# Performance work log

Measured on AMD Instinct MI355X. Metric: run time of the kernel, lower is better.

## Reference

```python
import jax, jax.numpy as jnp
import numpy as np
import math

NEIGHBOR_RADIUS = 30.0

def _masked_softmax(logits, mask, axis):
    # mask: bool, True = keep; all-masked rows return zeros
    p = jax.nn.softmax(jnp.where(mask, logits, -1e9), axis=axis) * mask.astype(logits.dtype)
    return p / jnp.clip(jnp.sum(p, axis=axis, keepdims=True), 1e-9, None)

def _forward(agents_state, agents_mask, map_polylines, map_poly_mask,
             map_poly_type, map_tl_status, map_on_route,
             pm_w1, pm_b1, pm_w2, pm_b2, type_emb, tl_emb, route_emb,
             mo_w1, mo_b1, mo_w2, mo_b2,
             ae_w1, ae_b1, ae_w2, ae_b2, ae_w3, ae_b3,
             mr_w1, mr_b1, mr_w2, mr_b2,
             nr_w1, nr_b1, nr_w2, nr_b2,
             to_w1, to_b1, to_w2, to_b2):
    relu = jax.nn.relu
    a_mask = (agents_mask > 0.5).astype(agents_state.dtype)   # (B,N,T)
    a_feat = agents_state[..., :5]
    # ---- map polyline node encoder ----
    h = relu(map_polylines @ pm_w1 + pm_b1)                   # (B,M,L,H)
    h = relu(h @ pm_w2 + pm_b2)
    h = h.max(axis=2)                                         # (B,M,H) max-pool over points
    t_idx = jnp.clip(map_poly_type, 0, type_emb.shape[0] - 1)
    s_idx = jnp.clip(map_tl_status, 0, tl_emb.shape[0] - 1)
    r_idx = jnp.clip(map_on_route, 0, route_emb.shape[0] - 1)
    h = h + type_emb[t_idx] + tl_emb[s_idx] + route_emb[r_idx]
    h = relu(h @ mo_w1 + mo_b1) @ mo_w2 + mo_b2
    map_mask = map_poly_mask > 0.5                            # (B,M) bool
    map_node = h * map_mask[..., None].astype(h.dtype)        # (B,M,D)
    map_center = map_polylines.mean(axis=2)                   # (B,M,2)
    # ---- agent state encoder ----
    a = relu(a_feat @ ae_w1 + ae_b1)
    a = relu(a @ ae_w2 + ae_b2)
    a_emb = (a @ ae_w3 + ae_b3) * a_mask[..., None]           # (B,N,T,D)
    D = a_emb.shape[-1]
    # ---- agent -> map attention ----
    agent_pos = a_feat[..., 0:2]
    rel = map_center[:, None, None, :, :] - agent_pos[:, :, :, None, :]  # (B,N,T,M,2)
    dist = jnp.linalg.norm(rel, axis=-1, keepdims=True)
    rel_feat = jnp.concatenate([rel, dist], axis=-1)          # (B,N,T,M,3)
    rel_score = (relu(rel_feat @ mr_w1 + mr_b1) @ mr_w2 + mr_b2)[..., 0]  # (B,N,T,M)
    dot = jnp.einsum('bntd,bmd->bntm', a_emb, map_node) / math.sqrt(D)
    score_mask = jnp.broadcast_to(map_mask[:, None, None, :], dot.shape)
    attn = _masked_softmax(dot + rel_score, score_mask, axis=-1)
    map_ctx = jnp.einsum('bntm,bmd->bntd', attn, map_node)    # (B,N,T,D)
    # ---- neighbor graph attention ----
    pos = a_feat[..., 0:2]
    vel = a_feat[..., 3:5]
    pos_j = jnp.transpose(pos, (0, 2, 1, 3))                  # (B,T,N,2)
    vel_j = jnp.transpose(vel, (0, 2, 1, 3))
    rel_pos = pos_j[:, None, :, :, :] - pos[:, :, :, None, :] # (B,N,T,N,2) = p_j - p_i
    rel_vel = vel_j[:, None, :, :, :] - vel[:, :, :, None, :]
    dist_ij = jnp.linalg.norm(rel_pos, axis=-1, keepdims=True)
    rel_ij = jnp.concatenate([rel_pos, rel_vel, dist_ij], axis=-1)        # (B,N,T,N,5)
    nbr_score = (relu(rel_ij @ nr_w1 + nr_b1) @ nr_w2 + nr_b2)[..., 0]    # (B,N,T,N)
    am_b = agents_mask > 0.5
    valid_i = am_b[..., None]                                 # (B,N,T,1)
    valid_j = jnp.transpose(am_b, (0, 2, 1))[:, None, :, :]   # (B,1,T,N)
    N = pos.shape[1]
    not_self = ~jnp.eye(N, dtype=bool)[None, :, None, :]      # (1,N,1,N)
    nbr_mask = valid_i & valid_j & (dist_ij[..., 0] <= NEIGHBOR_RADIUS) & not_self
    dot_n = jnp.einsum('bitd,bjtd->bitj', a_emb, a_emb) / math.sqrt(D)
    w_n = _masked_softmax(dot_n + nbr_score, nbr_mask, axis=-1)
    nbr_ctx = jnp.einsum('bitj,bjtd->bitd', w_n, a_emb)       # (B,N,T,D)
    # ---- tau head ----
    tau = jnp.concatenate([a_emb, map_ctx, nbr_ctx], axis=-1)
    tau = relu(tau @ to_w1 + to_b1) @ to_w2 + to_b2
    return tau * a_mask[..., None]

def setup_inputs() -> dict:
    key = jax.random.key(0)
    B, N, T, M, L = 2, 32, 32, 256, 20
    H, D, TAU = 128, 128, 64
    ks = jax.random.split(key, 32)
    def f(i, shp):
        return jax.random.normal(ks[i], shp, jnp.float32) * 0.05
    inp = {}
    inp['agents_state'] = jax.random.normal(ks[0], (B, N, T, 5), jnp.float32) * jnp.array([50., 50., 1., 5., 5.], jnp.float32)
    inp['agents_mask'] = jnp.ones((B, N, T), jnp.float32)
    inp['map_polylines'] = jax.random.normal(ks[1], (B, M, L, 2), jnp.float32) * 50.0
    inp['map_poly_mask'] = jnp.ones((B, M), jnp.float32)
    inp['map_poly_type'] = jax.random.randint(ks[2], (B, M), 0, 4)
    inp['map_tl_status'] = jax.random.randint(ks[3], (B, M), 0, 8)
    inp['map_on_route'] = jax.random.randint(ks[4], (B, M), 0, 2)
    inp['pm_w1'] = f(5, (2, H));  inp['pm_b1'] = jnp.zeros((H,), jnp.float32)
    inp['pm_w2'] = f(6, (H, H)); inp['pm_b2'] = jnp.zeros((H,), jnp.float32)
    inp['type_emb'] = f(7, (4, H)); inp['tl_emb'] = f(8, (8, H)); inp['route_emb'] = f(9, (2, H))
    inp['mo_w1'] = f(10, (H, H)); inp['mo_b1'] = jnp.zeros((H,), jnp.float32)
    inp['mo_w2'] = f(11, (H, D)); inp['mo_b2'] = jnp.zeros((D,), jnp.float32)
    inp['ae_w1'] = f(12, (5, H)); inp['ae_b1'] = jnp.zeros((H,), jnp.float32)
    inp['ae_w2'] = f(13, (H, H)); inp['ae_b2'] = jnp.zeros((H,), jnp.float32)
    inp['ae_w3'] = f(14, (H, D)); inp['ae_b3'] = jnp.zeros((D,), jnp.float32)
    inp['mr_w1'] = f(15, (3, H)); inp['mr_b1'] = jnp.zeros((H,), jnp.float32)
    inp['mr_w2'] = f(16, (H, 1)); inp['mr_b2'] = jnp.zeros((1,), jnp.float32)
    inp['nr_w1'] = f(17, (5, H)); inp['nr_b1'] = jnp.zeros((H,), jnp.float32)
    inp['nr_w2'] = f(18, (H, 1)); inp['nr_b2'] = jnp.zeros((1,), jnp.float32)
    inp['to_w1'] = f(19, (3 * D, H)); inp['to_b1'] = jnp.zeros((H,), jnp.float32)
    inp['to_w2'] = f(20, (H, TAU)); inp['to_b2'] = jnp.zeros((TAU,), jnp.float32)
    return inp

def reference(agents_state, agents_mask, map_polylines, map_poly_mask,
              map_poly_type, map_tl_status, map_on_route,
              pm_w1, pm_b1, pm_w2, pm_b2, type_emb, tl_emb, route_emb,
              mo_w1, mo_b1, mo_w2, mo_b2,
              ae_w1, ae_b1, ae_w2, ae_b2, ae_w3, ae_b3,
              mr_w1, mr_b1, mr_w2, mr_b2,
              nr_w1, nr_b1, nr_w2, nr_b2,
              to_w1, to_b1, to_w2, to_b2):
    return _forward(agents_state, agents_mask, map_polylines, map_poly_mask,
                    map_poly_type, map_tl_status, map_on_route,
                    pm_w1, pm_b1, pm_w2, pm_b2, type_emb, tl_emb, route_emb,
                    mo_w1, mo_b1, mo_w2, mo_b2,
                    ae_w1, ae_b1, ae_w2, ae_b2, ae_w3, ae_b3,
                    mr_w1, mr_b1, mr_w2, mr_b2,
                    nr_w1, nr_b1, nr_w2, nr_b2,
                    to_w1, to_b1, to_w2, to_b2)
```

## Files before the change

kernel.cpp:

```cpp
#include <hip/hip_runtime.h>
#include <hip/hip_bf16.h>

#define Bb 2
#define Nn 32
#define Tt 32
#define Mm 256
#define Ll 20
#define Hh 128
#define Dd 128
#define TAUu 64
#define RSQRT_D 0.08838834764831843f

__global__ __launch_bounds__(256) void k_map(
    const float* __restrict__ poly, const float* __restrict__ pmask,
    const int* __restrict__ ptype, const int* __restrict__ ptl, const int* __restrict__ proute,
    const float* __restrict__ pm_w1, const float* __restrict__ pm_b1,
    const float* __restrict__ pm_w2, const float* __restrict__ pm_b2,
    const float* __restrict__ type_emb, const float* __restrict__ tl_emb, const float* __restrict__ route_emb,
    const float* __restrict__ mo_w1, const float* __restrict__ mo_b1,
    const float* __restrict__ mo_w2, const float* __restrict__ mo_b2,
    float* __restrict__ map_node, float* __restrict__ map_nodeT, float* __restrict__ map_center)
{
    int bm = blockIdx.x;
    int b  = bm >> 8;
    int m  = bm & 255;
    int tid = threadIdx.x;
    int h    = tid & 127;
    int half = tid >> 7;
    __shared__ float pts[Ll*2];
    __shared__ float h1a[Ll][Hh];
    __shared__ float hv[Hh];
    __shared__ float red[Hh];
    if (tid < Ll*2) pts[tid] = poly[bm*Ll*2 + tid];
    __syncthreads();
    float w1x = pm_w1[h];
    float w1y = pm_w1[Hh+h];
    float bb1 = pm_b1[h];
    int l0 = half*10;
    #pragma unroll
    for (int u = 0; u < 10; ++u) {
        int l = l0 + u;
        h1a[l][h] = fmaxf(fmaf(w1x, pts[2*l], fmaf(w1y, pts[2*l+1], bb1)), 0.f);
    }
    __syncthreads();
    float bb2 = pm_b2[h];
    float acc[10];
    #pragma unroll
    for (int u = 0; u < 10; ++u) acc[u] = bb2;
    for (int k = 0; k < Hh; ++k) {
        float w = pm_w2[k*Hh + h];
        #pragma unroll
        for (int u = 0; u < 10; ++u) acc[u] = fmaf(h1a[l0+u][k], w, acc[u]);
    }
    float mx = 0.f;
    #pragma unroll
    for (int u = 0; u < 10; ++u) mx = fmaxf(mx, acc[u]);
    if (half == 1) red[h] = mx;
    __syncthreads();
    if (half == 0) {
        float mm2 = fmaxf(mx, red[h]);
        int ti = min(max(ptype[bm], 0), 3);
        int si = min(max(ptl[bm], 0), 7);
        int ri = min(max(proute[bm], 0), 1);
        hv[h] = mm2 + type_emb[ti*Hh+h] + tl_emb[si*Hh+h] + route_emb[ri*Hh+h];
    }
    __syncthreads();
    float a1 = 0.f;
    for (int k = half*64; k < half*64 + 64; ++k) a1 = fmaf(hv[k], mo_w1[k*Hh+h], a1);
    if (half == 1) red[h] = a1;
    __syncthreads();
    if (half == 0) hv[h] = fmaxf(a1 + red[h] + mo_b1[h], 0.f);
    __syncthreads();
    float a2 = 0.f;
    for (int k = half*64; k < half*64 + 64; ++k) a2 = fmaf(hv[k], mo_w2[k*Dd+h], a2);
    if (half == 1) red[h] = a2;
    __syncthreads();
    if (half == 0) {
        float val = a2 + red[h] + mo_b2[h];
        float mk = (pmask[bm] > 0.5f) ? 1.f : 0.f;
        val *= mk;
        map_node[bm*Dd + h] = val;
        map_nodeT[(b*Dd + h)*Mm + m] = val;
    }
    if (tid == 0) {
        float sx = 0.f, sy = 0.f;
        for (int l = 0; l < Ll; ++l) { sx += pts[2*l]; sy += pts[2*l+1]; }
        map_center[bm*2+0] = sx / (float)Ll;
        map_center[bm*2+1] = sy / (float)Ll;
    }
}

__global__ __launch_bounds__(128) void k_agent(
    const float* __restrict__ astate, const float* __restrict__ amask,
    const float* __restrict__ ae_w1, const float* __restrict__ ae_b1,
    const float* __restrict__ ae_w2, const float* __restrict__ ae_b2,
    const float* __restrict__ ae_w3, const float* __restrict__ ae_b3,
    float* __restrict__ a_emb)
{
    int r0 = blockIdx.x * 4;
    int h  = threadIdx.x;
    __shared__ float f5[4][5];
    __shared__ float a1s[4][Hh];
    if (h < 20) f5[h/5][h%5] = astate[(r0 + h/5)*5 + (h%5)];
    __syncthreads();
    float acc[4];
    float b1v = ae_b1[h];
    #pragma unroll
    for (int r = 0; r < 4; ++r) acc[r] = b1v;
    #pragma unroll
    for (int k = 0; k < 5; ++k) {
        float w = ae_w1[k*Hh + h];
        #pragma unroll
        for (int r = 0; r < 4; ++r) acc[r] = fmaf(f5[r][k], w, acc[r]);
    }
    #pragma unroll
    for (int r = 0; r < 4; ++r) a1s[r][h] = fmaxf(acc[r], 0.f);
    __syncthreads();
    float b2v = ae_b2[h];
    #pragma unroll
    for (int r = 0; r < 4; ++r) acc[r] = b2v;
    for (int k = 0; k < Hh; ++k) {
        float w = ae_w2[k*Hh + h];
        #pragma unroll
        for (int r = 0; r < 4; ++r) acc[r] = fmaf(a1s[r][k], w, acc[r]);
    }
    float v2[4];
    #pragma unroll
    for (int r = 0; r < 4; ++r) v2[r] = fmaxf(acc[r], 0.f);
    __syncthreads();
    #pragma unroll
    for (int r = 0; r < 4; ++r) a1s[r][h] = v2[r];
    __syncthreads();
    float b3v = ae_b3[h];
    #pragma unroll
    for (int r = 0; r < 4; ++r) acc[r] = b3v;
    for (int k = 0; k < Hh; ++k) {
        float w = ae_w3[k*Dd + h];
        #pragma unroll
        for (int r = 0; r < 4; ++r) acc[r] = fmaf(a1s[r][k], w, acc[r]);
    }
    #pragma unroll
    for (int r = 0; r < 4; ++r) {
        float mk = (amask[r0+r] > 0.5f) ? 1.f : 0.f;
        a_emb[(r0+r)*Dd + h] = acc[r] * mk;
    }
}

__global__ __launch_bounds__(256) void k_mapattn(
    const float* __restrict__ astate, const float* __restrict__ pmask,
    const float* __restrict__ a_emb, const float* __restrict__ map_node,
    const float* __restrict__ map_nodeT, const float* __restrict__ map_center,
    const float* __restrict__ mr_w1, const float* __restrict__ mr_b1,
    const float* __restrict__ mr_w2, const float* __restrict__ mr_b2,
    float* __restrict__ map_ctx)
{
    int r0  = blockIdx.x * 4;
    int b   = r0 >> 10;
    int tid = threadIdx.x;
    __shared__ float w1m[3*Hh];
    __shared__ float b1m[Hh];
    __shared__ float w2m[Hh];
    __shared__ float pxy4[4][2];
    __shared__ float ae4[4][Dd];
    __shared__ float lg4[4][Mm];
    __shared__ float redc[4][Dd];
    for (int q = tid; q < 3*Hh; q += 256) w1m[q] = mr_w1[q];
    if (tid < Hh) { b1m[tid] = mr_b1[tid]; w2m[tid] = mr_w2[tid]; }
    for (int q = tid; q < 512; q += 256) ae4[q>>7][q&127] = a_emb[(r0 + (q>>7))*Dd + (q&127)];
    if (tid < 8) pxy4[tid>>1][tid&1] = astate[(r0 + (tid>>1))*5 + (tid&1)];
    float b2c = mr_b2[0];
    __syncthreads();

    {
        int m = tid;
        float cx = map_center[(b*Mm+m)*2+0];
        float cy = map_center[(b*Mm+m)*2+1];
        float rx[4], ry[4], dv[4], sA[4], dt[4];
        #pragma unroll
        for (int r = 0; r < 4; ++r) {
            rx[r] = cx - pxy4[r][0];
            ry[r] = cy - pxy4[r][1];
            dv[r] = sqrtf(rx[r]*rx[r] + ry[r]*ry[r]);
            sA[r] = b2c;
            dt[r] = 0.f;
        }
        for (int hh = 0; hh < Hh; ++hh) {
            float wa = w1m[hh], wb = w1m[Hh+hh], wc = w1m[2*Hh+hh];
            float bbv = b1m[hh], w2v = w2m[hh];
            #pragma unroll
            for (int r = 0; r < 4; ++r) {
                float t1 = fmaxf(fmaf(rx[r], wa, fmaf(ry[r], wb, fmaf(dv[r], wc, bbv))), 0.f);
                sA[r] = fmaf(t1, w2v, sA[r]);
            }
        }
        for (int d = 0; d < Dd; ++d) {
            float v = map_nodeT[(b*Dd + d)*Mm + m];
            #pragma unroll
            for (int r = 0; r < 4; ++r) dt[r] = fmaf(ae4[r][d], v, dt[r]);
        }
        bool mk = pmask[b*Mm+m] > 0.5f;
        #pragma unroll
        for (int r = 0; r < 4; ++r)
            lg4[r][m] = mk ? fmaf(dt[r], RSQRT_D, sA[r]) : -1e30f;
    }
    __syncthreads();

    {
        int w = tid >> 6, lam = tid & 63;
        float x0 = lg4[w][lam], x1 = lg4[w][64+lam], x2 = lg4[w][128+lam], x3 = lg4[w][192+lam];
        float mxv = fmaxf(fmaxf(x0,x1), fmaxf(x2,x3));
        for (int off = 32; off; off >>= 1) mxv = fmaxf(mxv, __shfl_xor(mxv, off));
        float e0 = (x0 > -1e29f) ? expf(x0-mxv) : 0.f;
        float e1 = (x1 > -1e29f) ? expf(x1-mxv) : 0.f;
        float e2 = (x2 > -1e29f) ? expf(x2-mxv) : 0.f;
        float e3 = (x3 > -1e29f) ? expf(x3-mxv) : 0.f;
        float sm = e0+e1+e2+e3;
        for (int off = 32; off; off >>= 1) sm += __shfl_xor(sm, off);
        float inv = 1.f / fmaxf(sm, 1e-9f);
        lg4[w][lam]     = e0*inv;
        lg4[w][64+lam]  = e1*inv;
        lg4[w][128+lam] = e2*inv;
        lg4[w][192+lam] = e3*inv;
    }
    __syncthreads();

    {
        int d = tid & 127, hf = tid >> 7;
        float acc[4] = {0.f, 0.f, 0.f, 0.f};
        for (int mm = 0; mm < 128; ++mm) {
            int m2 = (hf<<7) + mm;
            float v = map_node[(b*Mm+m2)*Dd + d];
            #pragma unroll
            for (int r = 0; r < 4; ++r) acc[r] = fmaf(lg4[r][m2], v, acc[r]);
        }
        if (hf == 1) {
            #pragma unroll
            for (int r = 0; r < 4; ++r) redc[r][d] = acc[r];
        }
        __syncthreads();
        if (hf == 0) {
            #pragma unroll
            for (int r = 0; r < 4; ++r) map_ctx[(r0+r)*Dd + d] = acc[r] + redc[r][d];
        }
    }
}

__global__ __launch_bounds__(256) void k_nbr_out(
    const float* __restrict__ astate, const float* __restrict__ amask,
    const float* __restrict__ a_emb, const float* __restrict__ map_ctx,
    const float* __restrict__ nr_w1, const float* __restrict__ nr_b1,
    const float* __restrict__ nr_w2, const float* __restrict__ nr_b2,
    const float* __restrict__ to_w1, const float* __restrict__ to_b1,
    const float* __restrict__ to_w2, const float* __restrict__ to_b2,
    float* __restrict__ out)
{
    int r0 = blockIdx.x * 4;
    int b  = r0 >> 10;
    int i  = (r0 >> 5) & 31;
    int t0 = r0 & 31;
    int tid = threadIdx.x;
    __shared__ float w1n[5*Hh];
    __shared__ float b1n[Hh];
    __shared__ float w2n[Hh];
    __shared__ float ei4[4][Dd];
    __shared__ float tau[4][3*Dd];
    __shared__ float jdat[4][Nn][5];
    __shared__ float rowdat[4][5];
    __shared__ float lgn[4][Nn];
    __shared__ float g1s[4][Hh];
    __shared__ float redn[4][Dd];

    for (int q = tid; q < 5*Hh; q += 256) w1n[q] = nr_w1[q];
    if (tid < Hh) { b1n[tid] = nr_b1[tid]; w2n[tid] = nr_w2[tid]; }
    for (int q = tid; q < 512; q += 256) {
        int rr = q>>7, d = q&127;
        float v = a_emb[(r0+rr)*Dd + d];
        ei4[rr][d] = v;
        tau[rr][d] = v;
        tau[rr][Dd + d] = map_ctx[(r0+rr)*Dd + d];
    }
    if (tid < 128) {
        int rr = tid >> 5, j = tid & 31;
        int rj = ((b*Nn + j)*Tt + t0 + rr);
        jdat[rr][j][0] = astate[rj*5+0];
        jdat[rr][j][1] = astate[rj*5+1];
        jdat[rr][j][2] = astate[rj*5+3];
        jdat[rr][j][3] = astate[rj*5+4];
        jdat[rr][j][4] = amask[rj];
    }
    if (tid < 4) {
        int ri_ = r0 + tid;
        rowdat[tid][0] = astate[ri_*5+0];
        rowdat[tid][1] = astate[ri_*5+1];
        rowdat[tid][2] = astate[ri_*5+3];
        rowdat[tid][3] = astate[ri_*5+4];
        rowdat[tid][4] = amask[ri_];
    }
    float b2c = nr_b2[0];
    __syncthreads();

    {
        int j = tid >> 3, c = tid & 7;
        float mlp[4], dtn[4], ddv[4];
        #pragma unroll
        for (int r = 0; r < 4; ++r) {
            float rpx = jdat[r][j][0] - rowdat[r][0];
            float rpy = jdat[r][j][1] - rowdat[r][1];
            float rvx = jdat[r][j][2] - rowdat[r][2];
            float rvy = jdat[r][j][3] - rowdat[r][3];
            float dd = sqrtf(rpx*rpx + rpy*rpy);
            int rj = ((b*Nn + j)*Tt + t0 + r);
            const float* ej = a_emb + (size_t)rj*Dd;
            float am = 0.f, ad = 0.f;
            #pragma unroll 4
            for (int u = 0; u < 16; ++u) {
                int hh = (u<<3) + c;
                float t1 = fmaf(rpx, w1n[hh], fmaf(rpy, w1n[Hh+hh],
                           fmaf(rvx, w1n[2*Hh+hh], fmaf(rvy, w1n[3*Hh+hh],
                           fmaf(dd,  w1n[4*Hh+hh], b1n[hh])))));
                t1 = fmaxf(t1, 0.f);
                am = fmaf(t1, w2n[hh], am);
                ad = fmaf(ei4[r][hh], ej[hh], ad);
            }
            am += __shfl_xor(am, 1); ad += __shfl_xor(ad, 1);
            am += __shfl_xor(am, 2); ad += __shfl_xor(ad, 2);
            am += __shfl_xor(am, 4); ad += __shfl_xor(ad, 4);
            mlp[r] = am; dtn[r] = ad; ddv[r] = dd;
        }
        if (c == 0) {
            #pragma unroll
            for (int r = 0; r < 4; ++r) {
                bool vi = rowdat[r][4] > 0.5f;
                bool vj = jdat[r][j][4] > 0.5f;
                bool ok = vi && vj && (ddv[r] <= 30.0f) && (j != i);
                lgn[r][j] = ok ? fmaf(dtn[r], RSQRT_D, b2c + mlp[r]) : -1e30f;
            }
        }
    }
    __syncthreads();

    {
        int w = tid >> 6, lam = tid & 63;
        float x = (lam < Nn) ? lgn[w][lam] : -1e30f;
        float mxv = x;
        for (int off = 32; off; off >>= 1) mxv = fmaxf(mxv, __shfl_xor(mxv, off));
        float e = (x > -1e29f) ? expf(x - mxv) : 0.f;
        float sm = e;
        for (int off = 32; off; off >>= 1) sm += __shfl_xor(sm, off);
        float inv = 1.f / fmaxf(sm, 1e-9f);
        if (lam < Nn) lgn[w][lam] = e * inv;
    }
    __syncthreads();

    {
        int d = tid & 127, hf = tid >> 7;
        float acc[4] = {0.f,0.f,0.f,0.f};
        for (int jj = 0; jj < 16; ++jj) {
            int j2 = (hf<<4) + jj;
            #pragma unroll
            for (int r = 0; r < 4; ++r) {
                float v = a_emb[((size_t)((b*Nn + j2)*Tt + t0 + r))*Dd + d];
                acc[r] = fmaf(lgn[r][j2], v, acc[r]);
            }
        }
        if (hf == 1) {
            #pragma unroll
            for (int r = 0; r < 4; ++r) redn[r][d] = acc[r];
        }
        __syncthreads();
        if (hf == 0) {
            #pragma unroll
            for (int r = 0; r < 4; ++r) tau[r][2*Dd + d] = acc[r] + redn[r][d];
        }
    }
    __syncthreads();

    {
        int h = tid & 127, rp = tid >> 7;
        float accA = 0.f, accB = 0.f;
        for (int k = 0; k < 3*Dd; ++k) {
            float w = to_w1[k*Hh + h];
            accA = fmaf(tau[rp][k],   w, accA);
            accB = fmaf(tau[rp+2][k], w, accB);
        }
        float bv = to_b1[h];
        g1s[rp][h]   = fmaxf(accA + bv, 0.f);
        g1s[rp+2][h] = fmaxf(accB + bv, 0.f);
    }
    __syncthreads();

    {
        int o = tid & 63, row = tid >> 6;
        float acc = to_b2[o];
        for (int hh = 0; hh < Hh; ++hh) acc = fmaf(g1s[row][hh], to_w2[hh*TAUu + o], acc);
        float vi = (rowdat[row][4] > 0.5f) ? 1.f : 0.f;
        out[(r0+row)*TAUu + o] = acc * vi;
    }
}

extern "C" void kernel_launch(void* const* d_in, const int* in_sizes, int n_in,
                              void* d_out, int out_size, void* d_ws, size_t ws_size,
                              hipStream_t stream) {
    const float* agents_state  = (const float*)d_in[0];
    const float* agents_mask   = (const float*)d_in[1];
    const float* map_polylines = (const float*)d_in[2];
    const float* map_poly_mask = (const float*)d_in[3];
    const int*   map_poly_type = (const int*)d_in[4];
    const int*   map_tl_status = (const int*)d_in[5];
    const int*   map_on_route  = (const int*)d_in[6];
    const float* pm_w1 = (const float*)d_in[7];
    const float* pm_b1 = (const float*)d_in[8];
    const float* pm_w2 = (const float*)d_in[9];
    const float* pm_b2 = (const float*)d_in[10];
    const float* type_emb  = (const float*)d_in[11];
    const float* tl_emb    = (const float*)d_in[12];
    const float* route_emb = (const float*)d_in[13];
    const float* mo_w1 = (const float*)d_in[14];
    const float* mo_b1 = (const float*)d_in[15];
    const float* mo_w2 = (const float*)d_in[16];
    const float* mo_b2 = (const float*)d_in[17];
    const float* ae_w1 = (const float*)d_in[18];
    const float* ae_b1 = (const float*)d_in[19];
    const float* ae_w2 = (const float*)d_in[20];
    const float* ae_b2 = (const float*)d_in[21];
    const float* ae_w3 = (const float*)d_in[22];
    const float* ae_b3 = (const float*)d_in[23];
    const float* mr_w1 = (const float*)d_in[24];
    const float* mr_b1 = (const float*)d_in[25];
    const float* mr_w2 = (const float*)d_in[26];
    const float* mr_b2 = (const float*)d_in[27];
    const float* nr_w1 = (const float*)d_in[28];
    const float* nr_b1 = (const float*)d_in[29];
    const float* nr_w2 = (const float*)d_in[30];
    const float* nr_b2 = (const float*)d_in[31];
    const float* to_w1 = (const float*)d_in[32];
    const float* to_b1 = (const float*)d_in[33];
    const float* to_w2 = (const float*)d_in[34];
    const float* to_b2 = (const float*)d_in[35];

    float* ws = (float*)d_ws;
    float* map_node   = ws;
    float* map_nodeT  = ws + 65536;
    float* map_center = ws + 131072;
    float* a_emb      = ws + 132096;
    float* map_ctx    = ws + 394240;

    float* out = (float*)d_out;

    k_map<<<Bb*Mm, 256, 0, stream>>>(map_polylines, map_poly_mask,
        map_poly_type, map_tl_status, map_on_route,
        pm_w1, pm_b1, pm_w2, pm_b2, type_emb, tl_emb, route_emb,
        mo_w1, mo_b1, mo_w2, mo_b2, map_node, map_nodeT, map_center);

    k_agent<<<Bb*Nn*Tt/4, 128, 0, stream>>>(agents_state, agents_mask,
        ae_w1, ae_b1, ae_w2, ae_b2, ae_w3, ae_b3, a_emb);

    k_mapattn<<<Bb*Nn*Tt/4, 256, 0, stream>>>(agents_state, map_poly_mask,
        a_emb, map_node, map_nodeT, map_center, mr_w1, mr_b1, mr_w2, mr_b2, map_ctx);

    k_nbr_out<<<Bb*Nn*Tt/4, 256, 0, stream>>>(agents_state, agents_mask,
        a_emb, map_ctx, nr_w1, nr_b1, nr_w2, nr_b2,
        to_w1, to_b1, to_w2, to_b2, out);
}
```

Measured before the change: 202.4 us.

## Restructure pipeline into five kernels with split polyline MLP and merged attention

The map encoder is split in two. A fully parallel elementwise kernel computes the first polyline layer and the centers into a global buffer, and a second kernel does the second layer with register-blocked weights, the max-pool and the output MLP. Map attention and neighbor-score computation are merged into one launch with extra blocks, and the output MLP is split across four k-slices with float4 shared loads. Together these aim to raise parallelism and cut serial per-block work. The cost is a large intermediate buffer written and read through global memory, plus extra global traffic for the neighbor probabilities.

```diff
diff --git a/kernel.cpp b/kernel.cpp
--- a/kernel.cpp
+++ b/kernel.cpp
@@ -1,96 +1,30 @@
 #include <hip/hip_runtime.h>
-#include <hip/hip_bf16.h>
-
-#define Bb 2
-#define Nn 32
-#define Tt 32
-#define Mm 256
-#define Ll 20
-#define Hh 128
-#define Dd 128
-#define TAUu 64
+
 #define RSQRT_D 0.08838834764831843f
 
-__global__ __launch_bounds__(256) void k_map(
-    const float* __restrict__ poly, const float* __restrict__ pmask,
-    const int* __restrict__ ptype, const int* __restrict__ ptl, const int* __restrict__ proute,
+__global__ __launch_bounds__(256) void k1_poly(
+    const float* __restrict__ poly,
     const float* __restrict__ pm_w1, const float* __restrict__ pm_b1,
-    const float* __restrict__ pm_w2, const float* __restrict__ pm_b2,
-    const float* __restrict__ type_emb, const float* __restrict__ tl_emb, const float* __restrict__ route_emb,
-    const float* __restrict__ mo_w1, const float* __restrict__ mo_b1,
-    const float* __restrict__ mo_w2, const float* __restrict__ mo_b2,
-    float* __restrict__ map_node, float* __restrict__ map_nodeT, float* __restrict__ map_center)
+    float* __restrict__ h1g, float* __restrict__ center)
 {
-    int bm = blockIdx.x;
-    int b  = bm >> 8;
-    int m  = bm & 255;
-    int tid = threadIdx.x;
-    int h    = tid & 127;
-    int half = tid >> 7;
-    __shared__ float pts[Ll*2];
-    __shared__ float h1a[Ll][Hh];
-    __shared__ float hv[Hh];
-    __shared__ float red[Hh];
-    if (tid < Ll*2) pts[tid] = poly[bm*Ll*2 + tid];
-    __syncthreads();
-    float w1x = pm_w1[h];
-    float w1y = pm_w1[Hh+h];
-    float bb1 = pm_b1[h];
-    int l0 = half*10;
-    #pragma unroll
-    for (int u = 0; u < 10; ++u) {
-        int l = l0 + u;
-        h1a[l][h] = fmaxf(fmaf(w1x, pts[2*l], fmaf(w1y, pts[2*l+1], bb1)), 0.f);
-    }
-    __syncthreads();
-    float bb2 = pm_b2[h];
-    float acc[10];
-    #pragma unroll
-    for (int u = 0; u < 10; ++u) acc[u] = bb2;
-    for (int k = 0; k < Hh; ++k) {
-        float w = pm_w2[k*Hh + h];
-        #pragma unroll
-        for (int u = 0; u < 10; ++u) acc[u] = fmaf(h1a[l0+u][k], w, acc[u]);
-    }
-    float mx = 0.f;
-    #pragma unroll
-    for (int u = 0; u < 10; ++u) mx = fmaxf(mx, acc[u]);
-    if (half == 1) red[h] = mx;
-    __syncthreads();
-    if (half == 0) {
-        float mm2 = fmaxf(mx, red[h]);
-        int ti = min(max(ptype[bm], 0), 3);
-        int si = min(max(ptl[bm], 0), 7);
-        int ri = min(max(proute[bm], 0), 1);
-        hv[h] = mm2 + type_emb[ti*Hh+h] + tl_emb[si*Hh+h] + route_emb[ri*Hh+h];
-    }
-    __syncthreads();
-    float a1 = 0.f;
-    for (int k = half*64; k < half*64 + 64; ++k) a1 = fmaf(hv[k], mo_w1[k*Hh+h], a1);
-    if (half == 1) red[h] = a1;
-    __syncthreads();
-    if (half == 0) hv[h] = fmaxf(a1 + red[h] + mo_b1[h], 0.f);
-    __syncthreads();
-    float a2 = 0.f;
-    for (int k = half*64; k < half*64 + 64; ++k) a2 = fmaf(hv[k], mo_w2[k*Dd+h], a2);
-    if (half == 1) red[h] = a2;
-    __syncthreads();
-    if (half == 0) {
-        float val = a2 + red[h] + mo_b2[h];
-        float mk = (pmask[bm] > 0.5f) ? 1.f : 0.f;
-        val *= mk;
-        map_node[bm*Dd + h] = val;
-        map_nodeT[(b*Dd + h)*Mm + m] = val;
-    }
-    if (tid == 0) {
-        float sx = 0.f, sy = 0.f;
-        for (int l = 0; l < Ll; ++l) { sx += pts[2*l]; sy += pts[2*l+1]; }
-        map_center[bm*2+0] = sx / (float)Ll;
-        map_center[bm*2+1] = sy / (float)Ll;
-    }
-}
-
-__global__ __launch_bounds__(128) void k_agent(
+    int idx = blockIdx.x * 256 + threadIdx.x;
+    if (blockIdx.x < 5120) {
+        int row = idx >> 7, k = idx & 127;
+        float x = poly[row*2], y = poly[row*2+1];
+        h1g[idx] = fmaxf(fmaf(x, pm_w1[k], fmaf(y, pm_w1[128+k], pm_b1[k])), 0.f);
+    } else {
+        int p = idx - 5120*256;
+        if (p < 512) {
+            float sx = 0.f, sy = 0.f;
+            #pragma unroll
+            for (int l = 0; l < 20; ++l) { sx += poly[p*40 + 2*l]; sy += poly[p*40 + 2*l + 1]; }
+            center[p*2+0] = sx * 0.05f;
+            center[p*2+1] = sy * 0.05f;
+        }
+    }
+}
+
+__global__ __launch_bounds__(128) void k2_agent(
     const float* __restrict__ astate, const float* __restrict__ amask,
     const float* __restrict__ ae_w1, const float* __restrict__ ae_b1,
     const float* __restrict__ ae_w2, const float* __restrict__ ae_b2,
@@ -98,303 +32,361 @@
     float* __restrict__ a_emb)
 {
     int r0 = blockIdx.x * 4;
-    int h  = threadIdx.x;
+    int h = threadIdx.x;
     __shared__ float f5[4][5];
-    __shared__ float a1s[4][Hh];
+    __shared__ __align__(16) float a1s[4][128];
     if (h < 20) f5[h/5][h%5] = astate[(r0 + h/5)*5 + (h%5)];
     __syncthreads();
-    float acc[4];
     float b1v = ae_b1[h];
+    float v[4];
+    {
+        float w0 = ae_w1[h], w1 = ae_w1[128+h], w2 = ae_w1[256+h], w3 = ae_w1[384+h], w4 = ae_w1[512+h];
+        #pragma unroll
+        for (int r = 0; r < 4; ++r) {
+            float a = b1v;
+            a = fmaf(f5[r][0], w0, a); a = fmaf(f5[r][1], w1, a);
+            a = fmaf(f5[r][2], w2, a); a = fmaf(f5[r][3], w3, a);
+            a = fmaf(f5[r][4], w4, a);
+            v[r] = fmaxf(a, 0.f);
+        }
+    }
     #pragma unroll
-    for (int r = 0; r < 4; ++r) acc[r] = b1v;
+    for (int r = 0; r < 4; ++r) a1s[r][h] = v[r];
+    __syncthreads();
+    {
+        float b2v = ae_b2[h];
+        float a0 = b2v, a1 = b2v, a2 = b2v, a3 = b2v;
+        for (int kc = 0; kc < 32; ++kc) {
+            float4 x0 = *(const float4*)&a1s[0][kc*4];
+            float4 x1 = *(const float4*)&a1s[1][kc*4];
+            float4 x2 = *(const float4*)&a1s[2][kc*4];
+            float4 x3 = *(const float4*)&a1s[3][kc*4];
+            float w0 = ae_w2[(kc*4+0)*128+h], w1 = ae_w2[(kc*4+1)*128+h];
+            float w2 = ae_w2[(kc*4+2)*128+h], w3 = ae_w2[(kc*4+3)*128+h];
+            a0 = fmaf(x0.x,w0,fmaf(x0.y,w1,fmaf(x0.z,w2,fmaf(x0.w,w3,a0))));
+            a1 = fmaf(x1.x,w0,fmaf(x1.y,w1,fmaf(x1.z,w2,fmaf(x1.w,w3,a1))));
+            a2 = fmaf(x2.x,w0,fmaf(x2.y,w1,fmaf(x2.z,w2,fmaf(x2.w,w3,a2))));
+            a3 = fmaf(x3.x,w0,fmaf(x3.y,w1,fmaf(x3.z,w2,fmaf(x3.w,w3,a3))));
+        }
+        v[0]=fmaxf(a0,0.f); v[1]=fmaxf(a1,0.f); v[2]=fmaxf(a2,0.f); v[3]=fmaxf(a3,0.f);
+    }
+    __syncthreads();
     #pragma unroll
-    for (int k = 0; k < 5; ++k) {
-        float w = ae_w1[k*Hh + h];
-        #pragma unroll
-        for (int r = 0; r < 4; ++r) acc[r] = fmaf(f5[r][k], w, acc[r]);
-    }
-    #pragma unroll
-    for (int r = 0; r < 4; ++r) a1s[r][h] = fmaxf(acc[r], 0.f);
-    __syncthreads();
-    float b2v = ae_b2[h];
-    #pragma unroll
-    for (int r = 0; r < 4; ++r) acc[r] = b2v;
-    for (int k = 0; k < Hh; ++k) {
-        float w = ae_w2[k*Hh + h];
-        #pragma unroll
-        for (int r = 0; r < 4; ++r) acc[r] = fmaf(a1s[r][k], w, acc[r]);
-    }
-    float v2[4];
-    #pragma unroll
-    for (int r = 0; r < 4; ++r) v2[r] = fmaxf(acc[r], 0.f);
-    __syncthreads();
-    #pragma unroll
-    for (int r = 0; r < 4; ++r) a1s[r][h] = v2[r];
-    __syncthreads();
-    float b3v = ae_b3[h];
-    #pragma unroll
-    for (int r = 0; r < 4; ++r) acc[r] = b3v;
-    for (int k = 0; k < Hh; ++k) {
-        float w = ae_w3[k*Dd + h];
-        #pragma unroll
-        for (int r = 0; r < 4; ++r) acc[r] = fmaf(a1s[r][k], w, acc[r]);
+    for (int r = 0; r < 4; ++r) a1s[r][h] = v[r];
+    __syncthreads();
+    {
+        float b3v = ae_b3[h];
+        float a0 = b3v, a1 = b3v, a2 = b3v, a3 = b3v;
+        for (int kc = 0; kc < 32; ++kc) {
+            float4 x0 = *(const float4*)&a1s[0][kc*4];
+            float4 x1 = *(const float4*)&a1s[1][kc*4];
+            float4 x2 = *(const float4*)&a1s[2][kc*4];
+            float4 x3 = *(const float4*)&a1s[3][kc*4];
+            float w0 = ae_w3[(kc*4+0)*128+h], w1 = ae_w3[(kc*4+1)*128+h];
+            float w2 = ae_w3[(kc*4+2)*128+h], w3 = ae_w3[(kc*4+3)*128+h];
+            a0 = fmaf(x0.x,w0,fmaf(x0.y,w1,fmaf(x0.z,w2,fmaf(x0.w,w3,a0))));
+            a1 = fmaf(x1.x,w0,fmaf(x1.y,w1,fmaf(x1.z,w2,fmaf(x1.w,w3,a1))));
+            a2 = fmaf(x2.x,w0,fmaf(x2.y,w1,fmaf(x2.z,w2,fmaf(x2.w,w3,a2))));
+            a3 = fmaf(x3.x,w0,fmaf(x3.y,w1,fmaf(x3.z,w2,fmaf(x3.w,w3,a3))));
+        }
+        v[0]=a0; v[1]=a1; v[2]=a2; v[3]=a3;
     }
     #pragma unroll
     for (int r = 0; r < 4; ++r) {
         float mk = (amask[r0+r] > 0.5f) ? 1.f : 0.f;
-        a_emb[(r0+r)*Dd + h] = acc[r] * mk;
-    }
-}
-
-__global__ __launch_bounds__(256) void k_mapattn(
-    const float* __restrict__ astate, const float* __restrict__ pmask,
+        a_emb[(r0+r)*128 + h] = v[r] * mk;
+    }
+}
+
+__global__ __launch_bounds__(128) void k3_mapnode(
+    const float* __restrict__ h1g, const float* __restrict__ pmask,
+    const int* __restrict__ ptype, const int* __restrict__ ptl, const int* __restrict__ proute,
+    const float* __restrict__ pm_w2, const float* __restrict__ pm_b2,
+    const float* __restrict__ type_emb, const float* __restrict__ tl_emb, const float* __restrict__ route_emb,
+    const float* __restrict__ mo_w1, const float* __restrict__ mo_b1,
+    const float* __restrict__ mo_w2, const float* __restrict__ mo_b2,
+    float* __restrict__ map_node, float* __restrict__ map_nodeT)
+{
+    int bm = blockIdx.x;
+    int b = bm >> 8, m = bm & 255;
+    int h = threadIdx.x;
+    __shared__ __align__(16) float hv[128];
+    __shared__ __align__(16) float g2[128];
+    float acc[20];
+    #pragma unroll
+    for (int l = 0; l < 20; ++l) acc[l] = 0.f;
+    for (int kc = 0; kc < 8; ++kc) {
+        float w[16];
+        #pragma unroll
+        for (int i = 0; i < 16; ++i) w[i] = pm_w2[(kc*16+i)*128 + h];
+        const float* hb = h1g + bm*2560 + kc*16;
+        #pragma unroll
+        for (int l = 0; l < 20; ++l) {
+            const float* xl = hb + l*128;
+            #pragma unroll
+            for (int i = 0; i < 16; ++i) acc[l] = fmaf(xl[i], w[i], acc[l]);
+        }
+    }
+    float mx = acc[0];
+    #pragma unroll
+    for (int l = 1; l < 20; ++l) mx = fmaxf(mx, acc[l]);
+    float val = fmaxf(mx + pm_b2[h], 0.f);
+    int ti = min(max(ptype[bm],0),3);
+    int si = min(max(ptl[bm],0),7);
+    int ri = min(max(proute[bm],0),1);
+    hv[h] = val + type_emb[ti*128+h] + tl_emb[si*128+h] + route_emb[ri*128+h];
+    __syncthreads();
+    float a1 = mo_b1[h];
+    for (int kc = 0; kc < 32; ++kc) {
+        float4 xv = *(const float4*)&hv[kc*4];
+        a1 = fmaf(xv.x, mo_w1[(kc*4+0)*128+h],
+             fmaf(xv.y, mo_w1[(kc*4+1)*128+h],
+             fmaf(xv.z, mo_w1[(kc*4+2)*128+h],
+             fmaf(xv.w, mo_w1[(kc*4+3)*128+h], a1))));
+    }
+    g2[h] = fmaxf(a1, 0.f);
+    __syncthreads();
+    float a2 = mo_b2[h];
+    for (int kc = 0; kc < 32; ++kc) {
+        float4 xv = *(const float4*)&g2[kc*4];
+        a2 = fmaf(xv.x, mo_w2[(kc*4+0)*128+h],
+             fmaf(xv.y, mo_w2[(kc*4+1)*128+h],
+             fmaf(xv.z, mo_w2[(kc*4+2)*128+h],
+             fmaf(xv.w, mo_w2[(kc*4+3)*128+h], a2))));
+    }
+    float mk = (pmask[bm] > 0.5f) ? 1.f : 0.f;
+    a2 *= mk;
+    map_node[bm*128 + h] = a2;
+    map_nodeT[(b*128+h)*256 + m] = a2;
+}
+
+__global__ __launch_bounds__(256) void k4_attn(
+    const float* __restrict__ astate, const float* __restrict__ amask,
+    const float* __restrict__ pmask,
     const float* __restrict__ a_emb, const float* __restrict__ map_node,
-    const float* __restrict__ map_nodeT, const float* __restrict__ map_center,
+    const float* __restrict__ map_nodeT, const float* __restrict__ center,
     const float* __restrict__ mr_w1, const float* __restrict__ mr_b1,
     const float* __restrict__ mr_w2, const float* __restrict__ mr_b2,
-    float* __restrict__ map_ctx)
+    const float* __restrict__ nr_w1, const float* __restrict__ nr_b1,
+    const float* __restrict__ nr_w2, const float* __restrict__ nr_b2,
+    float* __restrict__ map_ctx, float* __restrict__ p_n)
 {
-    int r0  = blockIdx.x * 4;
-    int b   = r0 >> 10;
     int tid = threadIdx.x;
-    __shared__ float w1m[3*Hh];
-    __shared__ float b1m[Hh];
-    __shared__ float w2m[Hh];
-    __shared__ float pxy4[4][2];
-    __shared__ float ae4[4][Dd];
-    __shared__ float lg4[4][Mm];
-    __shared__ float redc[4][Dd];
-    for (int q = tid; q < 3*Hh; q += 256) w1m[q] = mr_w1[q];
-    if (tid < Hh) { b1m[tid] = mr_b1[tid]; w2m[tid] = mr_w2[tid]; }
-    for (int q = tid; q < 512; q += 256) ae4[q>>7][q&127] = a_emb[(r0 + (q>>7))*Dd + (q&127)];
-    if (tid < 8) pxy4[tid>>1][tid&1] = astate[(r0 + (tid>>1))*5 + (tid&1)];
-    float b2c = mr_b2[0];
-    __syncthreads();
-
-    {
+    int lam = tid & 63, wv = tid >> 6;
+    __shared__ float lg4[4][256];
+    __shared__ __align__(16) float p4[256*4];
+    __shared__ float ctxp[4][128];
+
+    if (blockIdx.x < 512) {
+        int r0 = blockIdx.x * 4;
+        int b = r0 >> 10;
         int m = tid;
-        float cx = map_center[(b*Mm+m)*2+0];
-        float cy = map_center[(b*Mm+m)*2+1];
-        float rx[4], ry[4], dv[4], sA[4], dt[4];
+        float rx[4], ry[4], dd[4], dt[4], sA[4];
+        float b2c = mr_b2[0];
+        float cx = center[(b*256+m)*2+0], cy = center[(b*256+m)*2+1];
         #pragma unroll
         for (int r = 0; r < 4; ++r) {
-            rx[r] = cx - pxy4[r][0];
-            ry[r] = cy - pxy4[r][1];
-            dv[r] = sqrtf(rx[r]*rx[r] + ry[r]*ry[r]);
-            sA[r] = b2c;
-            dt[r] = 0.f;
-        }
-        for (int hh = 0; hh < Hh; ++hh) {
-            float wa = w1m[hh], wb = w1m[Hh+hh], wc = w1m[2*Hh+hh];
-            float bbv = b1m[hh], w2v = w2m[hh];
+            float px = astate[(r0+r)*5+0], py = astate[(r0+r)*5+1];
+            rx[r] = cx - px; ry[r] = cy - py;
+            dd[r] = sqrtf(rx[r]*rx[r] + ry[r]*ry[r]);
+            dt[r] = 0.f; sA[r] = b2c;
+        }
+        #pragma unroll 8
+        for (int hh = 0; hh < 128; ++hh) {
+            float wa = mr_w1[hh], wb = mr_w1[128+hh], wc = mr_w1[256+hh];
+            float bb = mr_b1[hh], w2 = mr_w2[hh];
             #pragma unroll
             for (int r = 0; r < 4; ++r) {
-                float t1 = fmaxf(fmaf(rx[r], wa, fmaf(ry[r], wb, fmaf(dv[r], wc, bbv))), 0.f);
-                sA[r] = fmaf(t1, w2v, sA[r]);
+                float t1 = fmaf(rx[r], wa, fmaf(ry[r], wb, fmaf(dd[r], wc, bb)));
+                sA[r] = fmaf(fmaxf(t1, 0.f), w2, sA[r]);
             }
         }
-        for (int d = 0; d < Dd; ++d) {
-            float v = map_nodeT[(b*Dd + d)*Mm + m];
-            #pragma unroll
-            for (int r = 0; r < 4; ++r) dt[r] = fmaf(ae4[r][d], v, dt[r]);
-        }
-        bool mk = pmask[b*Mm+m] > 0.5f;
+        const float* mT = map_nodeT + b*128*256 + m;
+        #pragma unroll 8
+        for (int d = 0; d < 128; ++d) {
+            float v = mT[d*256];
+            #pragma unroll
+            for (int r = 0; r < 4; ++r)
+                dt[r] = fmaf(v, a_emb[(r0+r)*128 + d], dt[r]);
+        }
+        bool mk = pmask[b*256+m] > 0.5f;
         #pragma unroll
         for (int r = 0; r < 4; ++r)
             lg4[r][m] = mk ? fmaf(dt[r], RSQRT_D, sA[r]) : -1e30f;
-    }
-    __syncthreads();
-
-    {
-        int w = tid >> 6, lam = tid & 63;
-        float x0 = lg4[w][lam], x1 = lg4[w][64+lam], x2 = lg4[w][128+lam], x3 = lg4[w][192+lam];
-        float mxv = fmaxf(fmaxf(x0,x1), fmaxf(x2,x3));
-        for (int off = 32; off; off >>= 1) mxv = fmaxf(mxv, __shfl_xor(mxv, off));
-        float e0 = (x0 > -1e29f) ? expf(x0-mxv) : 0.f;
-        float e1 = (x1 > -1e29f) ? expf(x1-mxv) : 0.f;
-        float e2 = (x2 > -1e29f) ? expf(x2-mxv) : 0.f;
-        float e3 = (x3 > -1e29f) ? expf(x3-mxv) : 0.f;
-        float sm = e0+e1+e2+e3;
-        for (int off = 32; off; off >>= 1) sm += __shfl_xor(sm, off);
-        float inv = 1.f / fmaxf(sm, 1e-9f);
-        lg4[w][lam]     = e0*inv;
-        lg4[w][64+lam]  = e1*inv;
-        lg4[w][128+lam] = e2*inv;
-        lg4[w][192+lam] = e3*inv;
-    }
-    __syncthreads();
-
-    {
-        int d = tid & 127, hf = tid >> 7;
-        float acc[4] = {0.f, 0.f, 0.f, 0.f};
-        for (int mm = 0; mm < 128; ++mm) {
-            int m2 = (hf<<7) + mm;
-            float v = map_node[(b*Mm+m2)*Dd + d];
-            #pragma unroll
-            for (int r = 0; r < 4; ++r) acc[r] = fmaf(lg4[r][m2], v, acc[r]);
-        }
-        if (hf == 1) {
-            #pragma unroll
-            for (int r = 0; r < 4; ++r) redc[r][d] = acc[r];
-        }
         __syncthreads();
-        if (hf == 0) {
-            #pragma unroll
-            for (int r = 0; r < 4; ++r) map_ctx[(r0+r)*Dd + d] = acc[r] + redc[r][d];
-        }
-    }
-}
-
-__global__ __launch_bounds__(256) void k_nbr_out(
-    const float* __restrict__ astate, const float* __restrict__ amask,
-    const float* __restrict__ a_emb, const float* __restrict__ map_ctx,
-    const float* __restrict__ nr_w1, const float* __restrict__ nr_b1,
-    const float* __restrict__ nr_w2, const float* __restrict__ nr_b2,
+        {
+            float x0 = lg4[wv][lam], x1 = lg4[wv][64+lam], x2 = lg4[wv][128+lam], x3 = lg4[wv][192+lam];
+            float mxv = fmaxf(fmaxf(x0,x1), fmaxf(x2,x3));
+            #pragma unroll
+            for (int off = 32; off; off >>= 1) mxv = fmaxf(mxv, __shfl_xor(mxv, off));
+            float e0 = (x0 > -1e29f) ? expf(x0-mxv) : 0.f;
+            float e1 = (x1 > -1e29f) ? expf(x1-mxv) : 0.f;
+            float e2 = (x2 > -1e29f) ? expf(x2-mxv) : 0.f;
+            float e3 = (x3 > -1e29f) ? expf(x3-mxv) : 0.f;
+            float sm = e0+e1+e2+e3;
+            #pragma unroll
+            for (int off = 32; off; off >>= 1) sm += __shfl_xor(sm, off);
+            float inv = 1.f / fmaxf(sm, 1e-9f);
+            p4[lam*4 + wv]       = e0*inv;
+            p4[(64+lam)*4 + wv]  = e1*inv;
+            p4[(128+lam)*4 + wv] = e2*inv;
+            p4[(192+lam)*4 + wv] = e3*inv;
+        }
+        __syncthreads();
+        {
+            int d = tid & 127, hf = tid >> 7;
+            float ac0 = 0.f, ac1 = 0.f, ac2 = 0.f, ac3 = 0.f;
+            const float* mn = map_node + (b*256 + hf*128)*128 + d;
+            const float4* pp = (const float4*)p4 + hf*128;
+            #pragma unroll 4
+            for (int mm = 0; mm < 128; ++mm) {
+                float4 pv = pp[mm];
+                float v = mn[mm*128];
+                ac0 = fmaf(pv.x, v, ac0); ac1 = fmaf(pv.y, v, ac1);
+                ac2 = fmaf(pv.z, v, ac2); ac3 = fmaf(pv.w, v, ac3);
+            }
+            if (hf == 1) { ctxp[0][d]=ac0; ctxp[1][d]=ac1; ctxp[2][d]=ac2; ctxp[3][d]=ac3; }
+            __syncthreads();
+            if (hf == 0) {
+                map_ctx[(r0+0)*128+d] = ac0 + ctxp[0][d];
+                map_ctx[(r0+1)*128+d] = ac1 + ctxp[1][d];
+                map_ctx[(r0+2)*128+d] = ac2 + ctxp[2][d];
+                map_ctx[(r0+3)*128+d] = ac3 + ctxp[3][d];
+            }
+        }
+    } else {
+        int rA = (blockIdx.x - 512)*8 + wv*2;
+        int hf = lam >> 5, j = lam & 31;
+        int r = rA + hf;
+        int b = r >> 10, ii = (r >> 5) & 31, tt = r & 31;
+        int rj = (b*32 + j)*32 + tt;
+        float pxi = astate[r*5+0], pyi = astate[r*5+1], vxi = astate[r*5+3], vyi = astate[r*5+4];
+        float pxj = astate[rj*5+0], pyj = astate[rj*5+1], vxj = astate[rj*5+3], vyj = astate[rj*5+4];
+        float rpx = pxj-pxi, rpy = pyj-pyi, rvx = vxj-vxi, rvy = vyj-vyi;
+        float ddv = sqrtf(rpx*rpx + rpy*rpy);
+        float acc = nr_b2[0], dot = 0.f;
+        const float* ei = a_emb + (size_t)r*128;
+        const float* ej = a_emb + (size_t)rj*128;
+        #pragma unroll 8
+        for (int hh = 0; hh < 128; ++hh) {
+            float wA = nr_w1[hh], wB = nr_w1[128+hh], wC = nr_w1[256+hh];
+            float wD = nr_w1[384+hh], wE = nr_w1[512+hh];
+            float bb = nr_b1[hh], w2 = nr_w2[hh];
+            float t1 = fmaf(rpx, wA, fmaf(rpy, wB, fmaf(rvx, wC,
+                       fmaf(rvy, wD, fmaf(ddv, wE, bb)))));
+            acc = fmaf(fmaxf(t1, 0.f), w2, acc);
+            dot = fmaf(ei[hh], ej[hh], dot);
+        }
+        bool vi = amask[r] > 0.5f, vj = amask[rj] > 0.5f;
+        bool ok = vi && vj && (ddv <= 30.0f) && (j != ii);
+        float lg = ok ? fmaf(dot, RSQRT_D, acc) : -1e30f;
+        float mxv = lg;
+        #pragma unroll
+        for (int off = 16; off; off >>= 1) mxv = fmaxf(mxv, __shfl_xor(mxv, off));
+        float e = (lg > -1e29f) ? expf(lg - mxv) : 0.f;
+        float sm = e;
+        #pragma unroll
+        for (int off = 16; off; off >>= 1) sm += __shfl_xor(sm, off);
+        p_n[r*32 + j] = e / fmaxf(sm, 1e-9f);
+    }
+}
+
+__global__ __launch_bounds__(256) void k5_out(
+    const float* __restrict__ amask, const float* __restrict__ a_emb,
+    const float* __restrict__ map_ctx, const float* __restrict__ p_n,
     const float* __restrict__ to_w1, const float* __restrict__ to_b1,
     const float* __restrict__ to_w2, const float* __restrict__ to_b2,
     float* __restrict__ out)
 {
     int r0 = blockIdx.x * 4;
-    int b  = r0 >> 10;
-    int i  = (r0 >> 5) & 31;
-    int t0 = r0 & 31;
+    int b = r0 >> 10, t0 = r0 & 31;
     int tid = threadIdx.x;
-    __shared__ float w1n[5*Hh];
-    __shared__ float b1n[Hh];
-    __shared__ float w2n[Hh];
-    __shared__ float ei4[4][Dd];
-    __shared__ float tau[4][3*Dd];
-    __shared__ float jdat[4][Nn][5];
-    __shared__ float rowdat[4][5];
-    __shared__ float lgn[4][Nn];
-    __shared__ float g1s[4][Hh];
-    __shared__ float redn[4][Dd];
-
-    for (int q = tid; q < 5*Hh; q += 256) w1n[q] = nr_w1[q];
-    if (tid < Hh) { b1n[tid] = nr_b1[tid]; w2n[tid] = nr_w2[tid]; }
+    __shared__ __align__(16) float tau[4][384];
+    __shared__ float redn[4][128];
+    __shared__ __align__(16) float gpart[4][4][128];
+    __shared__ __align__(16) float g1s[4][128];
+
     for (int q = tid; q < 512; q += 256) {
-        int rr = q>>7, d = q&127;
-        float v = a_emb[(r0+rr)*Dd + d];
-        ei4[rr][d] = v;
-        tau[rr][d] = v;
-        tau[rr][Dd + d] = map_ctx[(r0+rr)*Dd + d];
-    }
-    if (tid < 128) {
-        int rr = tid >> 5, j = tid & 31;
-        int rj = ((b*Nn + j)*Tt + t0 + rr);
-        jdat[rr][j][0] = astate[rj*5+0];
-        jdat[rr][j][1] = astate[rj*5+1];
-        jdat[rr][j][2] = astate[rj*5+3];
-        jdat[rr][j][3] = astate[rj*5+4];
-        jdat[rr][j][4] = amask[rj];
-    }
-    if (tid < 4) {
-        int ri_ = r0 + tid;
-        rowdat[tid][0] = astate[ri_*5+0];
-        rowdat[tid][1] = astate[ri_*5+1];
-        rowdat[tid][2] = astate[ri_*5+3];
-        rowdat[tid][3] = astate[ri_*5+4];
-        rowdat[tid][4] = amask[ri_];
-    }
-    float b2c = nr_b2[0];
-    __syncthreads();
-
-    {
-        int j = tid >> 3, c = tid & 7;
-        float mlp[4], dtn[4], ddv[4];
-        #pragma unroll
-        for (int r = 0; r < 4; ++r) {
-            float rpx = jdat[r][j][0] - rowdat[r][0];
-            float rpy = jdat[r][j][1] - rowdat[r][1];
-            float rvx = jdat[r][j][2] - rowdat[r][2];
-            float rvy = jdat[r][j][3] - rowdat[r][3];
-            float dd = sqrtf(rpx*rpx + rpy*rpy);
-            int rj = ((b*Nn + j)*Tt + t0 + r);
-            const float* ej = a_emb + (size_t)rj*Dd;
-            float am = 0.f, ad = 0.f;
-            #pragma unroll 4
-            for (int u = 0; u < 16; ++u) {
-                int hh = (u<<3) + c;
-                float t1 = fmaf(rpx, w1n[hh], fmaf(rpy, w1n[Hh+hh],
-                           fmaf(rvx, w1n[2*Hh+hh], fmaf(rvy, w1n[3*Hh+hh],
-                           fmaf(dd,  w1n[4*Hh+hh], b1n[hh])))));
-                t1 = fmaxf(t1, 0.f);
-                am = fmaf(t1, w2n[hh], am);
-                ad = fmaf(ei4[r][hh], ej[hh], ad);
-            }
-            am += __shfl_xor(am, 1); ad += __shfl_xor(ad, 1);
-            am += __shfl_xor(am, 2); ad += __shfl_xor(ad, 2);
-            am += __shfl_xor(am, 4); ad += __shfl_xor(ad, 4);
-            mlp[r] = am; dtn[r] = ad; ddv[r] = dd;
-        }
-        if (c == 0) {
-            #pragma unroll
-            for (int r = 0; r < 4; ++r) {
-                bool vi = rowdat[r][4] > 0.5f;
-                bool vj = jdat[r][j][4] > 0.5f;
-                bool ok = vi && vj && (ddv[r] <= 30.0f) && (j != i);
-                lgn[r][j] = ok ? fmaf(dtn[r], RSQRT_D, b2c + mlp[r]) : -1e30f;
-            }
-        }
-    }
-    __syncthreads();
-
-    {
-        int w = tid >> 6, lam = tid & 63;
-        float x = (lam < Nn) ? lgn[w][lam] : -1e30f;
-        float mxv = x;
-        for (int off = 32; off; off >>= 1) mxv = fmaxf(mxv, __shfl_xor(mxv, off));
-        float e = (x > -1e29f) ? expf(x - mxv) : 0.f;
-        float sm = e;
-        for (int off = 32; off; off >>= 1) sm += __shfl_xor(sm, off);
-        float inv = 1.f / fmaxf(sm, 1e-9f);
-        if (lam < Nn) lgn[w][lam] = e * inv;
-    }
-    __syncthreads();
-
+        int rr = q >> 7, d = q & 127;
+        tau[rr][d]       = a_emb[(r0+rr)*128 + d];
+        tau[rr][128 + d] = map_ctx[(r0+rr)*128 + d];
+    }
+    __syncthreads();
     {
         int d = tid & 127, hf = tid >> 7;
-        float acc[4] = {0.f,0.f,0.f,0.f};
+        float ac[4] = {0.f,0.f,0.f,0.f};
         for (int jj = 0; jj < 16; ++jj) {
-            int j2 = (hf<<4) + jj;
-            #pragma unroll
-            for (int r = 0; r < 4; ++r) {
-                float v = a_emb[((size_t)((b*Nn + j2)*Tt + t0 + r))*Dd + d];
-                acc[r] = fmaf(lgn[r][j2], v, acc[r]);
-            }
-        }
-        if (hf == 1) {
-            #pragma unroll
-            for (int r = 0; r < 4; ++r) redn[r][d] = acc[r];
-        }
+            int j2 = hf*16 + jj;
+            float p0 = p_n[(r0+0)*32 + j2];
+            float p1 = p_n[(r0+1)*32 + j2];
+            float p2 = p_n[(r0+2)*32 + j2];
+            float p3 = p_n[(r0+3)*32 + j2];
+            const float* ejb = a_emb + (size_t)((b*32 + j2)*32 + t0)*128 + d;
+            ac[0] = fmaf(p0, ejb[0],     ac[0]);
+            ac[1] = fmaf(p1, ejb[128],   ac[1]);
+            ac[2] = fmaf(p2, ejb[256],   ac[2]);
+            ac[3] = fmaf(p3, ejb[384],   ac[3]);
+        }
+        if (hf == 1) { redn[0][d]=ac[0]; redn[1][d]=ac[1]; redn[2][d]=ac[2]; redn[3][d]=ac[3]; }
         __syncthreads();
         if (hf == 0) {
             #pragma unroll
-            for (int r = 0; r < 4; ++r) tau[r][2*Dd + d] = acc[r] + redn[r][d];
-        }
-    }
-    __syncthreads();
-
+            for (int r = 0; r < 4; ++r) tau[r][256 + d] = ac[r] + redn[r][d];
+        }
+    }
+    __syncthreads();
+    {
+        int h6 = tid & 63, kq = tid >> 6;
+        float aL[4] = {0.f,0.f,0.f,0.f};
+        float aH[4] = {0.f,0.f,0.f,0.f};
+        for (int c = 0; c < 24; ++c) {
+            int k4 = kq*24 + c;
+            float4 x0 = *(const float4*)&tau[0][k4*4];
+            float4 x1 = *(const float4*)&tau[1][k4*4];
+            float4 x2 = *(const float4*)&tau[2][k4*4];
+            float4 x3 = *(const float4*)&tau[3][k4*4];
+            float wl0 = to_w1[(k4*4+0)*128 + h6],    wh0 = to_w1[(k4*4+0)*128 + 64+h6];
+            float wl1 = to_w1[(k4*4+1)*128 + h6],    wh1 = to_w1[(k4*4+1)*128 + 64+h6];
+            float wl2 = to_w1[(k4*4+2)*128 + h6],    wh2 = to_w1[(k4*4+2)*128 + 64+h6];
+            float wl3 = to_w1[(k4*4+3)*128 + h6],    wh3 = to_w1[(k4*4+3)*128 + 64+h6];
+            aL[0]=fmaf(x0.x,wl0,fmaf(x0.y,wl1,fmaf(x0.z,wl2,fmaf(x0.w,wl3,aL[0]))));
+            aH[0]=fmaf(x0.x,wh0,fmaf(x0.y,wh1,fmaf(x0.z,wh2,fmaf(x0.w,wh3,aH[0]))));
+            aL[1]=fmaf(x1.x,wl0,fmaf(x1.y,wl1,fmaf(x1.z,wl2,fmaf(x1.w,wl3,aL[1]))));
+            aH[1]=fmaf(x1.x,wh0,fmaf(x1.y,wh1,fmaf(x1.z,wh2,fmaf(x1.w,wh3,aH[1]))));
+            aL[2]=fmaf(x2.x,wl0,fmaf(x2.y,wl1,fmaf(x2.z,wl2,fmaf(x2.w,wl3,aL[2]))));
+            aH[2]=fmaf(x2.x,wh0,fmaf(x2.y,wh1,fmaf(x2.z,wh2,fmaf(x2.w,wh3,aH[2]))));
+            aL[3]=fmaf(x3.x,wl0,fmaf(x3.y,wl1,fmaf(x3.z,wl2,fmaf(x3.w,wl3,aL[3]))));
+            aH[3]=fmaf(x3.x,wh0,fmaf(x3.y,wh1,fmaf(x3.z,wh2,fmaf(x3.w,wh3,aH[3]))));
+        }
+        #pragma unroll
+        for (int r = 0; r < 4; ++r) {
+            gpart[kq][r][h6]      = aL[r];
+            gpart[kq][r][64 + h6] = aH[r];
+        }
+    }
+    __syncthreads();
     {
         int h = tid & 127, rp = tid >> 7;
-        float accA = 0.f, accB = 0.f;
-        for (int k = 0; k < 3*Dd; ++k) {
-            float w = to_w1[k*Hh + h];
-            accA = fmaf(tau[rp][k],   w, accA);
-            accB = fmaf(tau[rp+2][k], w, accB);
-        }
         float bv = to_b1[h];
-        g1s[rp][h]   = fmaxf(accA + bv, 0.f);
-        g1s[rp+2][h] = fmaxf(accB + bv, 0.f);
-    }
-    __syncthreads();
-
+        #pragma unroll
+        for (int rr = rp; rr < 4; rr += 2) {
+            float s = gpart[0][rr][h] + gpart[1][rr][h] + gpart[2][rr][h] + gpart[3][rr][h];
+            g1s[rr][h] = fmaxf(s + bv, 0.f);
+        }
+    }
+    __syncthreads();
     {
         int o = tid & 63, row = tid >> 6;
-        float acc = to_b2[o];
-        for (int hh = 0; hh < Hh; ++hh) acc = fmaf(g1s[row][hh], to_w2[hh*TAUu + o], acc);
-        float vi = (rowdat[row][4] > 0.5f) ? 1.f : 0.f;
-        out[(r0+row)*TAUu + o] = acc * vi;
+        float a2 = to_b2[o];
+        for (int kc = 0; kc < 32; ++kc) {
+            float4 g = *(const float4*)&g1s[row][kc*4];
+            a2 = fmaf(g.x, to_w2[(kc*4+0)*64 + o],
+                 fmaf(g.y, to_w2[(kc*4+1)*64 + o],
+                 fmaf(g.z, to_w2[(kc*4+2)*64 + o],
+                 fmaf(g.w, to_w2[(kc*4+3)*64 + o], a2))));
+        }
+        float mk = (amask[r0+row] > 0.5f) ? 1.f : 0.f;
+        out[(r0+row)*64 + o] = a2 * mk;
     }
 }
 
@@ -439,26 +431,32 @@
     const float* to_b2 = (const float*)d_in[35];
 
     float* ws = (float*)d_ws;
-    float* map_node   = ws;
-    float* map_nodeT  = ws + 65536;
-    float* map_center = ws + 131072;
-    float* a_emb      = ws + 132096;
-    float* map_ctx    = ws + 394240;
+    float* h1g       = ws;
+    float* map_node  = ws + 1310720;
+    float* map_nodeT = ws + 1376256;
+    float* center    = ws + 1441792;
+    float* a_emb     = ws + 1442816;
+    float* map_ctx   = ws + 1704960;
+    float* p_n       = ws + 1967104;
 
     float* out = (float*)d_out;
 
-    k_map<<<Bb*Mm, 256, 0, stream>>>(map_polylines, map_poly_mask,
+    k1_poly<<<5122, 256, 0, stream>>>(map_polylines, pm_w1, pm_b1, h1g, center);
+
+    k2_agent<<<512, 128, 0, stream>>>(agents_state, agents_mask,
+        ae_w1, ae_b1, ae_w2, ae_b2, ae_w3, ae_b3, a_emb);
+
+    k3_mapnode<<<512, 128, 0, stream>>>(h1g, map_poly_mask,
         map_poly_type, map_tl_status, map_on_route,
-        pm_w1, pm_b1, pm_w2, pm_b2, type_emb, tl_emb, route_emb,
-        mo_w1, mo_b1, mo_w2, mo_b2, map_node, map_nodeT, map_center);
-
-    k_agent<<<Bb*Nn*Tt/4, 128, 0, stream>>>(agents_state, agents_mask,
-        ae_w1, ae_b1, ae_w2, ae_b2, ae_w3, ae_b3, a_emb);
-
-    k_mapattn<<<Bb*Nn*Tt/4, 256, 0, stream>>>(agents_state, map_poly_mask,
-        a_emb, map_node, map_nodeT, map_center, mr_w1, mr_b1, mr_w2, mr_b2, map_ctx);
-
-    k_nbr_out<<<Bb*Nn*Tt/4, 256, 0, stream>>>(agents_state, agents_mask,
-        a_emb, map_ctx, nr_w1, nr_b1, nr_w2, nr_b2,
+        pm_w2, pm_b2, type_emb, tl_emb, route_emb,
+        mo_w1, mo_b1, mo_w2, mo_b2, map_node, map_nodeT);
+
+    k4_attn<<<768, 256, 0, stream>>>(agents_state, agents_mask, map_poly_mask,
+        a_emb, map_node, map_nodeT, center,
+        mr_w1, mr_b1, mr_w2, mr_b2,
+        nr_w1, nr_b1, nr_w2, nr_b2,
+        map_ctx, p_n);
+
+    k5_out<<<512, 256, 0, stream>>>(agents_mask, a_emb, map_ctx, p_n,
         to_w1, to_b1, to_w2, to_b2, out);
 }
```

Result: slower. 227.3 us (+12.3%).
